# Performance work log

Measured on AMD Instinct MI355X. Metric: run time of the kernel, lower is better.

The kernel has to match this reference:

```python
import jax, jax.numpy as jnp
import numpy as np
import math

B, T, C = 4, 2048, 768
N_HEAD = 12
HEAD_DIM = C // N_HEAD


def setup_inputs() -> dict:
    key = jax.random.key(0)
    k1, k2, k3, k4, k5 = jax.random.split(key, 5)
    std = 0.02
    x = jax.random.normal(k1, (B, T, C), dtype=jnp.float32)
    W_attn = jax.random.normal(k2, (C, 3 * C), dtype=jnp.float32) * std
    b_attn = jnp.zeros((3 * C,), dtype=jnp.float32)
    W_proj = jax.random.normal(k3, (C, C), dtype=jnp.float32) * std
    b_proj = jnp.zeros((C,), dtype=jnp.float32)
    return {"x": x, "W_attn": W_attn, "b_attn": b_attn,
            "W_proj": W_proj, "b_proj": b_proj}


def reference(x, W_attn, b_attn, W_proj, b_proj):
    b, t, c = x.shape
    h, hd = N_HEAD, c // N_HEAD
    # qkv projection: [B,T,3C] -> q,k,v each [B,H,T,hd]
    qkv = x @ W_attn + b_attn
    qkv = qkv.reshape(b, t, 3, h, hd).transpose(2, 0, 3, 1, 4)  # [3,B,H,T,hd]
    q, k, v = qkv[0], qkv[1], qkv[2]
    scale = 1.0 / math.sqrt(hd)
    # full T x T attention scores (non-flash, as in original)
    attn = jnp.einsum('bhqd,bhkd->bhqk', q, k) * scale  # [B,H,T,T]
    causal = jnp.tril(jnp.ones((t, t), dtype=bool))
    attn = jnp.where(causal[None, None, :, :], attn, -jnp.inf)
    attn = jax.nn.softmax(attn, axis=-1)
    y = jnp.einsum('bhqk,bhkd->bhqd', attn, v)  # [B,H,T,hd]
    y = y.transpose(0, 2, 1, 3).reshape(b, t, c)  # merge heads
    return y @ W_proj + b_proj
```

## Files before the change

### kernel.cpp

```cpp
#include <hip/hip_runtime.h>
#include <hip/hip_bf16.h>
#include <cstdint>

#define B_  4
#define T_  2048
#define C_  768
#define H_  12
#define HD_ 64

#define AS1 __attribute__((address_space(1)))
#define AS3 __attribute__((address_space(3)))

typedef float    f32x4  __attribute__((ext_vector_type(4)));
typedef __bf16   bf16x8 __attribute__((ext_vector_type(8)));
typedef uint32_t u32x4  __attribute__((ext_vector_type(4)));

#define QSCL 0.18033688011112042f

__device__ __forceinline__ uint16_t f2b(float f) {
  __bf16 h = (__bf16)f;
  return __builtin_bit_cast(uint16_t, h);
}
__device__ __forceinline__ uint32_t pk2(float a, float b) {
  return (uint32_t)f2b(a) | ((uint32_t)f2b(b) << 16);
}

__global__ void k_cvt(const float* __restrict__ in, uint16_t* __restrict__ out, int n4) {
  int i = blockIdx.x * blockDim.x + threadIdx.x;
  if (i >= n4) return;
  float4 v = ((const float4*)in)[i];
  uint2 o;
  o.x = pk2(v.x, v.y);
  o.y = pk2(v.z, v.w);
  ((uint2*)out)[i] = o;
}

__global__ void k_tr2(const float* __restrict__ Wa, uint16_t* __restrict__ WtA,
                      const float* __restrict__ Wp, uint16_t* __restrict__ WtP) {
  __shared__ float tile[32][33];
  const int bx = blockIdx.x;
  const float* in;
  uint16_t* out;
  int Cc, n0;
  if (bx < 72) { in = Wa; out = WtA; Cc = 2304; n0 = bx * 32; }
  else         { in = Wp; out = WtP; Cc = 768;  n0 = (bx - 72) * 32; }
  const int k0 = blockIdx.y * 32;
  const int tx = threadIdx.x, ty = threadIdx.y;
#pragma unroll
  for (int i = 0; i < 32; i += 8)
    tile[ty + i][tx] = in[(size_t)(k0 + ty + i) * Cc + n0 + tx];
  __syncthreads();
#pragma unroll
  for (int i = 0; i < 32; i += 8)
    out[(size_t)(n0 + ty + i) * 768 + k0 + tx] = f2b(tile[tx][ty + i]);
}

template <int EPI>
__global__ __launch_bounds__(256, 3) void k_gemm(
    const uint16_t* __restrict__ A, const uint16_t* __restrict__ Bt,
    const float* __restrict__ bias, float* __restrict__ outF,
    uint16_t* __restrict__ outQKV, int M, int N, int K, int nY) {
  __shared__ __align__(16) uint16_t As[3][128 * 32];
  __shared__ __align__(16) uint16_t Bs[3][128 * 32];
  const int nwg = gridDim.x;
  const int bid = blockIdx.x;
  const int wgid = (bid & 7) * (nwg >> 3) + (bid >> 3);
  const int wy = wgid % nY, wx = wgid / nY;

  const int tid  = threadIdx.x;
  const int lane = tid & 63;
  const int wave = tid >> 6;
  const int wrow = (wave >> 1) * 64, wcol = (wave & 1) * 64;
  const int rowBase = wx * 128, colBase = wy * 128;
  const int l16 = lane & 15, kg = lane >> 4;

  f32x4 acc[4][4];
#pragma unroll
  for (int i = 0; i < 4; ++i)
#pragma unroll
    for (int j = 0; j < 4; ++j) acc[i][j] = (f32x4){0.f, 0.f, 0.f, 0.f};

  const int srow  = lane >> 2;
  const int sslot = lane & 3;
  const int ssw   = (sslot ^ (srow & 3)) << 3;

  auto STAGE = [&](int buf, int k0) {
#pragma unroll
    for (int i = 0; i < 2; ++i) {
      const int r = i * 64 + wave * 16 + srow;
      const uint16_t* srcA = A  + (size_t)(rowBase + r) * K + k0 + ssw;
      const uint16_t* srcB = Bt + (size_t)(colBase + r) * K + k0 + ssw;
      uint16_t* dstA = &As[buf][(i * 64 + wave * 16) * 32];
      uint16_t* dstB = &Bs[buf][(i * 64 + wave * 16) * 32];
      __builtin_amdgcn_global_load_lds((const AS1 uint32_t*)srcA, (AS3 uint32_t*)dstA, 16, 0, 0);
      __builtin_amdgcn_global_load_lds((const AS1 uint32_t*)srcB, (AS3 uint32_t*)dstB, 16, 0, 0);
    }
  };

  const int sA = (kg ^ (l16 & 3)) << 3;

  STAGE(0, 0);
  if (32 < K) STAGE(1, 32);
  int t = 0;
  for (int k0 = 0; k0 < K; k0 += 32, ++t) {
    if (k0 + 32 < K) {
      asm volatile("s_waitcnt vmcnt(4)" ::: "memory");
    } else {
      asm volatile("s_waitcnt vmcnt(0)" ::: "memory");
    }
    __builtin_amdgcn_sched_barrier(0);
    __builtin_amdgcn_s_barrier();

    if (k0 + 64 < K) STAGE((t + 2) % 3, k0 + 64);

    const int cb = t % 3;
    bf16x8 af[4], bfv[4];
#pragma unroll
    for (int mi = 0; mi < 4; ++mi)
      af[mi] = *(const bf16x8*)&As[cb][(wrow + mi * 16 + l16) * 32 + sA];
#pragma unroll
    for (int nj = 0; nj < 4; ++nj)
      bfv[nj] = *(const bf16x8*)&Bs[cb][(wcol + nj * 16 + l16) * 32 + sA];
#pragma unroll
    for (int mi = 0; mi < 4; ++mi)
#pragma unroll
      for (int nj = 0; nj < 4; ++nj)
        acc[mi][nj] = __builtin_amdgcn_mfma_f32_16x16x32_bf16(af[mi], bfv[nj], acc[mi][nj], 0, 0, 0);
  }

  const int rg = lane >> 4;
#pragma unroll
  for (int mi = 0; mi < 4; ++mi)
#pragma unroll
    for (int nj = 0; nj < 4; ++nj) {
      int c = colBase + wcol + nj * 16 + l16;
      float bv = bias[c];
      if (EPI == 0) {
#pragma unroll
        for (int jj = 0; jj < 4; ++jj) {
          int r = rowBase + wrow + mi * 16 + rg * 4 + jj;
          outF[(size_t)r * N + c] = acc[mi][nj][jj] + bv;
        }
      } else {
        int sel = c / 768;
        int rem = c - sel * 768;
        int head = rem >> 6, d = rem & 63;
        int r0 = rowBase + wrow + mi * 16 + rg * 4;
        int bb = r0 >> 11, tt0 = r0 & 2047;
        if (sel == 2) {
          size_t off = (((size_t)2 * (B_ * H_) + bb * H_ + head) * HD_ + d) * T_ + tt0;
          uint2 w;
          w.x = pk2(acc[mi][nj][0] + bv, acc[mi][nj][1] + bv);
          w.y = pk2(acc[mi][nj][2] + bv, acc[mi][nj][3] + bv);
          *(uint2*)&outQKV[off] = w;
        } else {
          float scl = (sel == 0) ? QSCL : 1.0f;
#pragma unroll
          for (int jj = 0; jj < 4; ++jj) {
            size_t off = (((size_t)sel * (B_ * H_) + bb * H_ + head) * T_ + tt0 + jj) * HD_ + d;
            outQKV[off] = f2b((acc[mi][nj][jj] + bv) * scl);
          }
        }
      }
    }
}

__global__ __launch_bounds__(512, 6) void k_attn2(
    const uint16_t* __restrict__ Qb, const uint16_t* __restrict__ Kb,
    const uint16_t* __restrict__ Vb, uint16_t* __restrict__ Y) {
  __shared__ __align__(16) uint16_t Ks[2][64 * 64];
  __shared__ __align__(16) uint16_t Vs[2][64 * 64];
  __shared__ __align__(16) uint32_t Pw[8][16 * 20];
  const int tid  = threadIdx.x;
  const int lane = tid & 63;
  const int wq   = tid >> 6;
  const int qw   = wq & 3;
  const int kh   = wq >> 2;
  const int l16  = lane & 15, kg = lane >> 4;

  const int idx = blockIdx.x;
  const int tq  = idx >> 3;
  const int px  = tq & 15;
  const int g   = (idx & 7) + 8 * (tq >> 4);
  const int h = g % H_, b = g / H_;
  const size_t headBase = ((size_t)(b * H_ + h)) * (size_t)(T_ * HD_);

  const int srow0 = tid >> 3;
  const int sslot = lane & 7;
  const int ssw   = ((sslot ^ (srow0 & 7)) << 3);

  uint32_t* pw = &Pw[wq][0];
  uint16_t* dstK0 = &Ks[0][(wq * 8) * 64];
  uint16_t* dstK1 = &Ks[1][(wq * 8) * 64];
  uint16_t* dstV0 = &Vs[0][(wq * 8) * 64];
  uint16_t* dstV1 = &Vs[1][(wq * 8) * 64];

  u32x4 onesw;
  onesw[0] = 0x3f803f80u; onesw[1] = 0x3f803f80u;
  onesw[2] = 0x3f803f80u; onesw[3] = 0x3f803f80u;
  const bf16x8 onesf = __builtin_bit_cast(bf16x8, onesw);

  int cur = 0;
  for (int part = 0; part < 2; ++part) {
    const int qb = part ? (31 - px) : px;
    const int qrow0 = qb * 64 + qw * 16;

    bf16x8 qf[2];
    {
      const uint16_t* qp = Qb + headBase + (size_t)(qrow0 + l16) * HD_;
      qf[0] = *(const bf16x8*)(qp + kg * 8);
      qf[1] = *(const bf16x8*)(qp + 32 + kg * 8);
    }

    f32x4 o[4];
#pragma unroll
    for (int i = 0; i < 4; ++i) o[i] = (f32x4){0.f, 0.f, 0.f, 0.f};
    f32x4 lq = (f32x4){0.f, 0.f, 0.f, 0.f};

    const uint16_t* kp = Kb + headBase + (size_t)srow0 * HD_ + ssw;
    const uint16_t* vp = Vb + headBase + (size_t)srow0 * T_ + ssw;

    auto STAGE = [&](int buf) {
      __builtin_amdgcn_global_load_lds((const AS1 uint32_t*)kp,
                                       (AS3 uint32_t*)(buf ? dstK1 : dstK0), 16, 0, 0);
      __builtin_amdgcn_global_load_lds((const AS1 uint32_t*)vp,
                                       (AS3 uint32_t*)(buf ? dstV1 : dstV0), 16, 0, 0);
      kp += 64 * HD_;
      vp += 64;
    };

    const int nt = qb + 1;
    __syncthreads();
    STAGE(cur);

    for (int t = 0; t < nt; ++t) {
      asm volatile("s_waitcnt vmcnt(0)" ::: "memory");
      __builtin_amdgcn_sched_barrier(0);
      __builtin_amdgcn_s_barrier();

      if (t + 1 < nt) STAGE(cur ^ 1);

      const uint16_t* KT = &Ks[cur][0];
      const uint16_t* VT = &Vs[cur][0];

      f32x4 sm[2];
      __builtin_amdgcn_s_setprio(1);
#pragma unroll
      for (int nj = 0; nj < 2; ++nj) {
        f32x4 acc = (f32x4){0.f, 0.f, 0.f, 0.f};
        const int row = kh * 32 + nj * 16 + l16;
#pragma unroll
        for (int kc = 0; kc < 2; ++kc) {
          const int s = (((kc * 4 + kg) ^ (row & 7)) << 3);
          bf16x8 kf = *(const bf16x8*)&KT[row * 64 + s];
          acc = __builtin_amdgcn_mfma_f32_16x16x32_bf16(kf, qf[kc], acc, 0, 0, 0);
        }
        sm[nj] = acc;
      }
      __builtin_amdgcn_s_setprio(0);

      if (t == qb) {
        const int kvb = t * 64 + kh * 32 + kg * 4;
        const int qg  = qrow0 + l16;
#pragma unroll
        for (int nj = 0; nj < 2; ++nj)
#pragma unroll
          for (int jj = 0; jj < 4; ++jj)
            if (kvb + nj * 16 + jj > qg) sm[nj][jj] = -__builtin_inff();
      }

#pragma unroll
      for (int nj = 0; nj < 2; ++nj)
#pragma unroll
        for (int jj = 0; jj < 4; ++jj)
          sm[nj][jj] = __builtin_exp2f(sm[nj][jj]);

#pragma unroll
      for (int nj = 0; nj < 2; ++nj) {
        uint2 w;
        w.x = pk2(sm[nj][0], sm[nj][1]);
        w.y = pk2(sm[nj][2], sm[nj][3]);
        *(uint2*)&pw[l16 * 20 + nj * 8 + kg * 2] = w;
      }

      __builtin_amdgcn_s_setprio(1);
      bf16x8 pa = *(const bf16x8*)&pw[l16 * 20 + kg * 4];
#pragma unroll
      for (int njd = 0; njd < 4; ++njd) {
        const int row = njd * 16 + l16;
        const int s = (((kh * 4 + kg) ^ (row & 7)) << 3);
        bf16x8 vf = *(const bf16x8*)&VT[row * 64 + s];
        o[njd] = __builtin_amdgcn_mfma_f32_16x16x32_bf16(vf, pa, o[njd], 0, 0, 0);
      }
      lq = __builtin_amdgcn_mfma_f32_16x16x32_bf16(onesf, pa, lq, 0, 0, 0);
      __builtin_amdgcn_s_setprio(0);

      cur ^= 1;
    }

    float l_ = lq[0];

    __syncthreads();
    f32x4* cO = (f32x4*)&Ks[0][0];
    float*  cL = (float*)&Vs[0][0];
    if (kh) {
#pragma unroll
      for (int njd = 0; njd < 4; ++njd) cO[(njd * 4 + qw) * 64 + lane] = o[njd];
      if (lane < 16) cL[qw * 64 + lane] = l_;
    }
    __syncthreads();
    if (!kh) {
      float lsum = l_ + cL[qw * 64 + l16];
      float inv = __builtin_amdgcn_rcpf(lsum);
      const int q = qrow0 + l16;
      uint16_t* yp = Y + ((size_t)(b * T_ + q)) * C_ + h * HD_ + kg * 4;
#pragma unroll
      for (int njd = 0; njd < 4; ++njd) {
        f32x4 oc = o[njd] + cO[(njd * 4 + qw) * 64 + lane];
        uint2 w;
        w.x = pk2(oc[0] * inv, oc[1] * inv);
        w.y = pk2(oc[2] * inv, oc[3] * inv);
        *(uint2*)(yp + njd * 16) = w;
      }
    }
  }
}

extern "C" void kernel_launch(void* const* d_in, const int* in_sizes, int n_in,
                              void* d_out, int out_size, void* d_ws, size_t ws_size,
                              hipStream_t stream) {
  const float* x      = (const float*)d_in[0];
  const float* W_attn = (const float*)d_in[1];
  const float* b_attn = (const float*)d_in[2];
  const float* W_proj = (const float*)d_in[3];
  const float* b_proj = (const float*)d_in[4];
  float* out = (float*)d_out;

  char* ws = (char*)d_ws;
  uint16_t* xb  = (uint16_t*)(ws);
  uint16_t* WtA = (uint16_t*)(ws + 12582912);
  uint16_t* WtP = (uint16_t*)(ws + 16121856);
  uint16_t* QKV = (uint16_t*)(ws + 17301504);
  uint16_t* Yb  = (uint16_t*)(ws + 55050240);

  uint16_t* Qp = QKV;
  uint16_t* Kp = QKV + 6291456;
  uint16_t* Vp = QKV + 12582912;

  k_cvt<<<6144, 256, 0, stream>>>(x, xb, 1572864);
  k_tr2<<<dim3(96, 24), dim3(32, 8), 0, stream>>>(W_attn, WtA, W_proj, WtP);
  k_gemm<1><<<1152, 256, 0, stream>>>(xb, WtA, b_attn, nullptr, QKV, 8192, 2304, 768, 18);
  k_attn2<<<768, 512, 0, stream>>>(Qp, Kp, Vp, Yb);
  k_gemm<0><<<384, 256, 0, stream>>>(Yb, WtP, b_proj, out, nullptr, 8192, 768, 768, 6);
}
```

Baseline: 132.5 us.

## Process 128-key tiles per iteration in attention with single-buffered LDS

The attention loop now handles 128 keys per iteration instead of 64. Each wave group computes four 16-key score blocks and does two PV MFMA passes, and the P scratch uses an XOR swizzle in place of padding. The K/V double buffer and its prefetch are replaced by a single larger buffer that is loaded and waited on at the top of each iteration. This halves the number of barriers and loop iterations, but gives up in-block load/compute overlap. It also wastes half a tile of fully masked work on diagonal blocks with an even index, and it adds an extra sync at the end of each part.

```diff
diff --git a/kernel.cpp b/kernel.cpp
--- a/kernel.cpp
+++ b/kernel.cpp
@@ -168,15 +168,16 @@
 __global__ __launch_bounds__(512, 6) void k_attn2(
     const uint16_t* __restrict__ Qb, const uint16_t* __restrict__ Kb,
     const uint16_t* __restrict__ Vb, uint16_t* __restrict__ Y) {
-  __shared__ __align__(16) uint16_t Ks[2][64 * 64];
-  __shared__ __align__(16) uint16_t Vs[2][64 * 64];
-  __shared__ __align__(16) uint32_t Pw[8][16 * 20];
+  __shared__ __align__(16) uint16_t Ks[128 * 64];
+  __shared__ __align__(16) uint16_t Vs[64 * 128];
+  __shared__ __align__(16) uint32_t Pw[8][16 * 32];
   const int tid  = threadIdx.x;
   const int lane = tid & 63;
   const int wq   = tid >> 6;
   const int qw   = wq & 3;
   const int kh   = wq >> 2;
   const int l16  = lane & 15, kg = lane >> 4;
+  const int l7   = l16 & 7;
 
   const int idx = blockIdx.x;
   const int tq  = idx >> 3;
@@ -185,22 +186,29 @@
   const int h = g % H_, b = g / H_;
   const size_t headBase = ((size_t)(b * H_ + h)) * (size_t)(T_ * HD_);
 
-  const int srow0 = tid >> 3;
-  const int sslot = lane & 7;
-  const int ssw   = ((sslot ^ (srow0 & 7)) << 3);
+  const int krow  = tid >> 3;
+  const int kslot = tid & 7;
+  const int vrow  = tid >> 4;
+  const int vslot = tid & 15;
+
+  const int swz = l7 << 2;
 
   uint32_t* pw = &Pw[wq][0];
-  uint16_t* dstK0 = &Ks[0][(wq * 8) * 64];
-  uint16_t* dstK1 = &Ks[1][(wq * 8) * 64];
-  uint16_t* dstV0 = &Vs[0][(wq * 8) * 64];
-  uint16_t* dstV1 = &Vs[1][(wq * 8) * 64];
+  uint16_t* dstK0 = &Ks[(wq * 8) * 64];
+  uint16_t* dstK1 = &Ks[(64 + wq * 8) * 64];
+  uint16_t* dstV0 = &Vs[(wq * 4) * 128];
+  uint16_t* dstV1 = &Vs[(32 + wq * 4) * 128];
 
   u32x4 onesw;
   onesw[0] = 0x3f803f80u; onesw[1] = 0x3f803f80u;
   onesw[2] = 0x3f803f80u; onesw[3] = 0x3f803f80u;
   const bf16x8 onesf = __builtin_bit_cast(bf16x8, onesw);
 
-  int cur = 0;
+  const uint16_t* kpA = Kb + headBase + (size_t)krow * HD_ + ((kslot ^ (krow & 7)) << 3);
+  const uint16_t* kpB = Kb + headBase + (size_t)(64 + krow) * HD_ + ((kslot ^ ((64 + krow) & 7)) << 3);
+  const uint16_t* vpA = Vb + headBase + (size_t)vrow * T_ + ((vslot ^ (vrow & 7)) << 3);
+  const uint16_t* vpB = Vb + headBase + (size_t)(32 + vrow) * T_ + ((vslot ^ ((32 + vrow) & 7)) << 3);
+
   for (int part = 0; part < 2; ++part) {
     const int qb = part ? (31 - px) : px;
     const int qrow0 = qb * 64 + qw * 16;
@@ -217,92 +225,85 @@
     for (int i = 0; i < 4; ++i) o[i] = (f32x4){0.f, 0.f, 0.f, 0.f};
     f32x4 lq = (f32x4){0.f, 0.f, 0.f, 0.f};
 
-    const uint16_t* kp = Kb + headBase + (size_t)srow0 * HD_ + ssw;
-    const uint16_t* vp = Vb + headBase + (size_t)srow0 * T_ + ssw;
-
-    auto STAGE = [&](int buf) {
-      __builtin_amdgcn_global_load_lds((const AS1 uint32_t*)kp,
-                                       (AS3 uint32_t*)(buf ? dstK1 : dstK0), 16, 0, 0);
-      __builtin_amdgcn_global_load_lds((const AS1 uint32_t*)vp,
-                                       (AS3 uint32_t*)(buf ? dstV1 : dstV0), 16, 0, 0);
-      kp += 64 * HD_;
-      vp += 64;
-    };
-
-    const int nt = qb + 1;
-    __syncthreads();
-    STAGE(cur);
+    const int nt = (qb >> 1) + 1;
 
     for (int t = 0; t < nt; ++t) {
+      __builtin_amdgcn_s_barrier();
+      {
+        const size_t koff = (size_t)(t * 128) * HD_;
+        const size_t voff = (size_t)(t * 128);
+        __builtin_amdgcn_global_load_lds((const AS1 uint32_t*)(kpA + koff), (AS3 uint32_t*)dstK0, 16, 0, 0);
+        __builtin_amdgcn_global_load_lds((const AS1 uint32_t*)(kpB + koff), (AS3 uint32_t*)dstK1, 16, 0, 0);
+        __builtin_amdgcn_global_load_lds((const AS1 uint32_t*)(vpA + voff), (AS3 uint32_t*)dstV0, 16, 0, 0);
+        __builtin_amdgcn_global_load_lds((const AS1 uint32_t*)(vpB + voff), (AS3 uint32_t*)dstV1, 16, 0, 0);
+      }
       asm volatile("s_waitcnt vmcnt(0)" ::: "memory");
       __builtin_amdgcn_sched_barrier(0);
       __builtin_amdgcn_s_barrier();
 
-      if (t + 1 < nt) STAGE(cur ^ 1);
-
-      const uint16_t* KT = &Ks[cur][0];
-      const uint16_t* VT = &Vs[cur][0];
-
-      f32x4 sm[2];
+      f32x4 sm[4];
       __builtin_amdgcn_s_setprio(1);
 #pragma unroll
-      for (int nj = 0; nj < 2; ++nj) {
+      for (int nj = 0; nj < 4; ++nj) {
         f32x4 acc = (f32x4){0.f, 0.f, 0.f, 0.f};
-        const int row = kh * 32 + nj * 16 + l16;
+        const int row = kh * 64 + nj * 16 + l16;
 #pragma unroll
         for (int kc = 0; kc < 2; ++kc) {
-          const int s = (((kc * 4 + kg) ^ (row & 7)) << 3);
-          bf16x8 kf = *(const bf16x8*)&KT[row * 64 + s];
+          const int s = (((kc * 4 + kg) ^ l7) << 3);
+          bf16x8 kf = *(const bf16x8*)&Ks[row * 64 + s];
           acc = __builtin_amdgcn_mfma_f32_16x16x32_bf16(kf, qf[kc], acc, 0, 0, 0);
         }
         sm[nj] = acc;
       }
       __builtin_amdgcn_s_setprio(0);
 
-      if (t == qb) {
-        const int kvb = t * 64 + kh * 32 + kg * 4;
+      if (t == nt - 1) {
+        const int kvb = t * 128 + kh * 64 + kg * 4;
         const int qg  = qrow0 + l16;
 #pragma unroll
-        for (int nj = 0; nj < 2; ++nj)
+        for (int nj = 0; nj < 4; ++nj)
 #pragma unroll
           for (int jj = 0; jj < 4; ++jj)
             if (kvb + nj * 16 + jj > qg) sm[nj][jj] = -__builtin_inff();
       }
 
 #pragma unroll
-      for (int nj = 0; nj < 2; ++nj)
+      for (int nj = 0; nj < 4; ++nj)
 #pragma unroll
         for (int jj = 0; jj < 4; ++jj)
           sm[nj][jj] = __builtin_exp2f(sm[nj][jj]);
 
 #pragma unroll
-      for (int nj = 0; nj < 2; ++nj) {
+      for (int nj = 0; nj < 4; ++nj) {
         uint2 w;
         w.x = pk2(sm[nj][0], sm[nj][1]);
         w.y = pk2(sm[nj][2], sm[nj][3]);
-        *(uint2*)&pw[l16 * 20 + nj * 8 + kg * 2] = w;
+        const int cs = (nj * 8 + kg * 2) ^ swz;
+        *(uint2*)&pw[l16 * 32 + cs] = w;
       }
 
       __builtin_amdgcn_s_setprio(1);
-      bf16x8 pa = *(const bf16x8*)&pw[l16 * 20 + kg * 4];
-#pragma unroll
-      for (int njd = 0; njd < 4; ++njd) {
-        const int row = njd * 16 + l16;
-        const int s = (((kh * 4 + kg) ^ (row & 7)) << 3);
-        bf16x8 vf = *(const bf16x8*)&VT[row * 64 + s];
-        o[njd] = __builtin_amdgcn_mfma_f32_16x16x32_bf16(vf, pa, o[njd], 0, 0, 0);
-      }
-      lq = __builtin_amdgcn_mfma_f32_16x16x32_bf16(onesf, pa, lq, 0, 0, 0);
+#pragma unroll
+      for (int kc = 0; kc < 2; ++kc) {
+        const int cr = (kc * 16 + kg * 4) ^ swz;
+        bf16x8 pa = *(const bf16x8*)&pw[l16 * 32 + cr];
+#pragma unroll
+        for (int njd = 0; njd < 4; ++njd) {
+          const int row = njd * 16 + l16;
+          const int s = (((kh * 8 + kc * 4 + kg) ^ l7) << 3);
+          bf16x8 vf = *(const bf16x8*)&Vs[row * 128 + s];
+          o[njd] = __builtin_amdgcn_mfma_f32_16x16x32_bf16(vf, pa, o[njd], 0, 0, 0);
+        }
+        lq = __builtin_amdgcn_mfma_f32_16x16x32_bf16(onesf, pa, lq, 0, 0, 0);
+      }
       __builtin_amdgcn_s_setprio(0);
-
-      cur ^= 1;
     }
 
     float l_ = lq[0];
 
     __syncthreads();
-    f32x4* cO = (f32x4*)&Ks[0][0];
-    float*  cL = (float*)&Vs[0][0];
+    f32x4* cO = (f32x4*)&Ks[0];
+    float*  cL = (float*)&Vs[0];
     if (kh) {
 #pragma unroll
       for (int njd = 0; njd < 4; ++njd) cO[(njd * 4 + qw) * 64 + lane] = o[njd];
@@ -323,6 +324,7 @@
         *(uint2*)(yp + njd * 16) = w;
       }
     }
+    __syncthreads();
   }
 }
 
```

After: 139.2 us. 5.1% more time.
